# Optimization experiments

Hardware: AMD Instinct MI355X
Metric: run time of the kernel (lower is better)

Reference implementation:

```python
import jax, jax.numpy as jnp
import numpy as np

B, L, D, NH = 4, 1024, 1024, 16
DH = D // NH
H = 8 * D // 3  # SwiGLU hidden = 2730
NEG = -1e9


def setup_inputs() -> dict:
    key = jax.random.key(0)
    ks = jax.random.split(key, 8)
    init = lambda k, shape: (jax.random.normal(k, shape, jnp.float32) * 0.02)
    x = jax.random.normal(ks[0], (B, L, D), jnp.float32)
    causal = jnp.tril(jnp.ones((L, L), bool))
    m = jnp.where(causal, 0.0, NEG)[None, None].astype(jnp.float32)  # [1,1,L,L]
    return {
        'x': x,
        'm': m,
        'wx': init(ks[1], (D, 3 * D)),
        'bx': jnp.zeros((3 * D,), jnp.float32),
        'wo': init(ks[2], (D, D)),
        'bo': jnp.zeros((D,), jnp.float32),
        'mhanorm_w': jnp.ones((D,), jnp.float32),
        'ffnorm_w': jnp.ones((D,), jnp.float32),
        'u': init(ks[3], (D, H)),
        'v': init(ks[4], (D, H)),
        'w': init(ks[5], (H, D)),
    }


def rmsnorm(x, weight, eps=1e-8):
    rrms = jax.lax.rsqrt(jnp.mean(x * x, axis=-1, keepdims=True) + eps)
    return weight * x * rrms


def reference(x, m, wx, bx, wo, bo, mhanorm_w, ffnorm_w, u, v, w):
    scale = D ** (-0.5)  # note: original uses d**-0.5, NOT dh**-0.5
    qkv = rmsnorm(x, mhanorm_w) @ wx + bx                 # [B,L,3D]
    q, k, vv = jnp.split(qkv, 3, axis=-1)                  # each [B,L,D]
    split = lambda t: t.reshape(B, L, NH, DH).transpose(0, 2, 1, 3)  # [B,NH,L,DH]
    q, k, vv = split(q), split(k), split(vv)               # pe = identity (default)
    scores = jnp.einsum('bhic,bhjc->bhij', q, k) * scale + m
    A = jax.nn.softmax(scores, axis=-1)
    head = jnp.einsum('bhij,bhjc->bhic', A, vv)            # [B,NH,L,DH]
    head = head.transpose(0, 2, 1, 3).reshape(B, L, D)
    x = x + head @ wo + bo
    xn = rmsnorm(x, ffnorm_w)
    return x + (jax.nn.silu(xn @ u) * (xn @ v)) @ w
```

## Files before the change

kernel.cpp:

```cpp
#include <hip/hip_runtime.h>

#define B_  4
#define L_  1024
#define D_  1024
#define NH_ 16
#define DH_ 64
#define H_  2730
#define HP_ 2816
#define M_  4096

typedef short bf16x8 __attribute__((ext_vector_type(8)));
typedef float f32x4  __attribute__((ext_vector_type(4)));

__device__ __forceinline__ unsigned short f2bf(float f) {
    unsigned int u = __builtin_bit_cast(unsigned int, f);
    u += 0x7fffu + ((u >> 16) & 1u);
    return (unsigned short)(u >> 16);
}
__device__ __forceinline__ float bf2f(unsigned short s) {
    unsigned int u = ((unsigned int)s) << 16;
    return __builtin_bit_cast(float, u);
}

__device__ __forceinline__ void glds16(const void* g, void* l) {
    __builtin_amdgcn_global_load_lds(
        (const __attribute__((address_space(1))) unsigned int*)g,
        (__attribute__((address_space(3))) unsigned int*)l, 16, 0, 0);
}

__device__ __forceinline__ void xcd_swz(int& lx, int& ly) {
    const int gx = gridDim.x;
    const int flat = blockIdx.x + gx * blockIdx.y;
    const int r = flat & 7, q = flat >> 3;
    lx = q % gx;
    ly = r + 8 * (q / gx);
}

__global__ __launch_bounds__(256) void cvtT_rms_all(
    const float* __restrict__ wx, const float* __restrict__ wo,
    const float* __restrict__ u,  const float* __restrict__ v,
    const float* __restrict__ w,
    const float* __restrict__ x,  const float* __restrict__ mhw,
    unsigned short* __restrict__ wxb, unsigned short* __restrict__ wob,
    unsigned short* __restrict__ ub,  unsigned short* __restrict__ vb,
    unsigned short* __restrict__ wb,  unsigned short* __restrict__ xnb)
{
    __shared__ float t[32][33];
    __shared__ float red[4];
    const int id = blockIdx.x;

    if (id >= 12544) {
        const int row = id - 12544;
        const int tt = threadIdx.x;
        const float4 vv = ((const float4*)(x + (size_t)row * 1024))[tt];
        float ss = vv.x*vv.x + vv.y*vv.y + vv.z*vv.z + vv.w*vv.w;
        #pragma unroll
        for (int off = 32; off > 0; off >>= 1) ss += __shfl_down(ss, off);
        if ((tt & 63) == 0) red[tt >> 6] = ss;
        __syncthreads();
        const float tot = red[0] + red[1] + red[2] + red[3];
        const float rr = rsqrtf(tot * (1.0f / 1024.0f) + 1e-8f);
        const float4 wv = ((const float4*)mhw)[tt];
        ushort4 o;
        o.x = f2bf(vv.x * wv.x * rr); o.y = f2bf(vv.y * wv.y * rr);
        o.z = f2bf(vv.z * wv.z * rr); o.w = f2bf(vv.w * wv.w * rr);
        ((ushort4*)(xnb + (size_t)row * 1024))[tt] = o;
        return;
    }

    const float* in; unsigned short* out;
    int K, N, Kp, gx, base;
    if (id < 3072)      { in = wx; out = wxb; K = 1024; N = 3072; Kp = 1024; gx = 32; base = 0; }
    else if (id < 4096) { in = wo; out = wob; K = 1024; N = 1024; Kp = 1024; gx = 32; base = 3072; }
    else if (id < 6912) { in = u;  out = ub;  K = 1024; N = 2730; Kp = 1024; gx = 32; base = 4096; }
    else if (id < 9728) { in = v;  out = vb;  K = 1024; N = 2730; Kp = 1024; gx = 32; base = 6912; }
    else                { in = w;  out = wb;  K = 2730; N = 1024; Kp = 2816; gx = 88; base = 9728; }
    const int local = id - base;
    const int bx = local % gx, by = local / gx;

    const int k0 = bx * 32, n0 = by * 32;
    const int tx = threadIdx.x & 31, ty = threadIdx.x >> 5;
    #pragma unroll
    for (int i = 0; i < 4; ++i) {
        const int k = k0 + ty + i * 8, n = n0 + tx;
        t[ty + i * 8][tx] = (k < K && n < N) ? in[(size_t)k * N + n] : 0.0f;
    }
    __syncthreads();
    #pragma unroll
    for (int i = 0; i < 4; ++i) {
        const int n = n0 + ty + i * 8, k = k0 + tx;
        out[(size_t)n * Kp + k] = f2bf(t[tx][ty + i * 8]);
    }
}

__global__ __launch_bounds__(256) void rmsnorm_kernel(
    const float* __restrict__ x, const float* __restrict__ w,
    unsigned short* __restrict__ out)
{
    const int row = blockIdx.x;
    const int t = threadIdx.x;
    const float4 v = ((const float4*)(x + (size_t)row * 1024))[t];
    float ss = v.x*v.x + v.y*v.y + v.z*v.z + v.w*v.w;
    #pragma unroll
    for (int off = 32; off > 0; off >>= 1) ss += __shfl_down(ss, off);
    __shared__ float red[4];
    if ((t & 63) == 0) red[t >> 6] = ss;
    __syncthreads();
    const float tot = red[0] + red[1] + red[2] + red[3];
    const float rr = rsqrtf(tot * (1.0f / 1024.0f) + 1e-8f);
    const float4 wv = ((const float4*)w)[t];
    ushort4 o;
    o.x = f2bf(v.x * wv.x * rr); o.y = f2bf(v.y * wv.y * rr);
    o.z = f2bf(v.z * wv.z * rr); o.w = f2bf(v.w * wv.w * rr);
    ((ushort4*)(out + (size_t)row * 1024))[t] = o;
}

template<int EPI, int TN>
__global__ __launch_bounds__(256) void gemm_bf16(
    const unsigned short* __restrict__ A, const unsigned short* __restrict__ Bt,
    int M, int N, int K,
    const float* __restrict__ bias, const float* __restrict__ res,
    float* __restrict__ outf, unsigned short* __restrict__ outb)
{
    constexpr int NS = TN / 32;
    constexpr int G  = (TN == 128) ? 4 : 3;
    constexpr int WAIT_G = 0xF70 | G;
    __shared__ __align__(16) unsigned short As[2][128 * 32];
    __shared__ __align__(16) unsigned short Bs[2][TN * 32];
    const int tid = threadIdx.x;
    int lx, ly;
    xcd_swz(lx, ly);
    const int m0 = ly * 128, n0 = lx * TN;
    const int lane = tid & 63, w = tid >> 6;
    const int wm = w >> 1, wn = w & 1;
    const int quad = lane >> 4, l15 = lane & 15;

    f32x4 acc[4][NS] = {};

    const int p0 = w * 64 + lane;
    const int r0 = p0 >> 2, c0 = (p0 & 3) ^ ((r0 >> 1) & 3);
    const int offL0 = p0 * 8, offL1 = 2048 + p0 * 8;

    const unsigned short* Ag0 = A + (size_t)(m0 + r0) * K + c0 * 8;
    const unsigned short* Ag1 = A + (size_t)(m0 + 64 + r0) * K + c0 * 8;
    const unsigned short* Bg0 = Bt + (size_t)(n0 + r0) * K + c0 * 8;
    const unsigned short* Bg1 = Bt + (size_t)(n0 + 64 + r0) * K + c0 * 8;

    auto stage = [&](int kk, int buf) {
        glds16(Ag0 + kk, &As[buf][offL0]);
        glds16(Ag1 + kk, &As[buf][offL1]);
        glds16(Bg0 + kk, &Bs[buf][offL0]);
        if (TN == 128) glds16(Bg1 + kk, &Bs[buf][offL1]);
    };
    auto compute = [&](int buf) {
        bf16x8 af[4], bfr[NS];
        #pragma unroll
        for (int ms = 0; ms < 4; ++ms) {
            const int row = wm * 64 + ms * 16 + l15;
            af[ms] = *(const bf16x8*)&As[buf][row * 32 + ((quad ^ ((row >> 1) & 3)) * 8)];
        }
        #pragma unroll
        for (int ns = 0; ns < NS; ++ns) {
            const int row = wn * (TN / 2) + ns * 16 + l15;
            bfr[ns] = *(const bf16x8*)&Bs[buf][row * 32 + ((quad ^ ((row >> 1) & 3)) * 8)];
        }
        #pragma unroll
        for (int ms = 0; ms < 4; ++ms)
            #pragma unroll
            for (int ns = 0; ns < NS; ++ns)
                acc[ms][ns] = __builtin_amdgcn_mfma_f32_16x16x32_bf16(
                    af[ms], bfr[ns], acc[ms][ns], 0, 0, 0);
    };

    const int nk = K >> 5;
    stage(0, 0);
    for (int i = 0; i < nk; i += 2) {
        if (i + 1 < nk) { stage((i + 1) << 5, 1); __builtin_amdgcn_s_waitcnt(WAIT_G); }
        else            { __builtin_amdgcn_s_waitcnt(0xF70); }
        __builtin_amdgcn_s_barrier();
        compute(0);
        __builtin_amdgcn_s_barrier();
        if (i + 2 < nk) { stage((i + 2) << 5, 0); __builtin_amdgcn_s_waitcnt(WAIT_G); }
        else            { __builtin_amdgcn_s_waitcnt(0xF70); }
        __builtin_amdgcn_s_barrier();
        compute(1);
        __builtin_amdgcn_s_barrier();
    }

    #pragma unroll
    for (int ms = 0; ms < 4; ++ms) {
        #pragma unroll
        for (int r = 0; r < 4; ++r) {
            const int row = m0 + wm * 64 + ms * 16 + quad * 4 + r;
            const size_t ro = (size_t)row * N;
            #pragma unroll
            for (int ns = 0; ns < NS; ++ns) {
                const int col = n0 + wn * (TN / 2) + ns * 16 + l15;
                float v = acc[ms][ns][r];
                if (EPI == 0) {
                    outb[ro + col] = f2bf(v + bias[col]);
                } else if (EPI == 1) {
                    outf[ro + col] = v + bias[col] + res[ro + col];
                } else {
                    outf[ro + col] = v + res[ro + col];
                }
            }
        }
    }
}

__global__ __launch_bounds__(256, 2) void gemm_swiglu(
    const unsigned short* __restrict__ A, const unsigned short* __restrict__ Bu,
    const unsigned short* __restrict__ Bv, unsigned short* __restrict__ g)
{
    constexpr int K = 1024, N = HP_;
    constexpr int WAIT_G = 0xF76;
    __shared__ __align__(16) unsigned short As[2][128 * 32];
    __shared__ __align__(16) unsigned short Us[2][128 * 32];
    __shared__ __align__(16) unsigned short Vs[2][128 * 32];
    const int tid = threadIdx.x;
    int lx, ly;
    xcd_swz(lx, ly);
    const int m0 = ly * 128, n0 = lx * 128;
    const int lane = tid & 63, w = tid >> 6;
    const int wm = w >> 1, wn = w & 1;
    const int quad = lane >> 4, l15 = lane & 15;

    f32x4 au[4][4] = {}, av[4][4] = {};

    const int p0 = w * 64 + lane;
    const int r0 = p0 >> 2, c0 = (p0 & 3) ^ ((r0 >> 1) & 3);
    const int offL0 = p0 * 8, offL1 = 2048 + p0 * 8;

    const unsigned short* Ag0 = A  + (size_t)(m0 + r0) * K + c0 * 8;
    const unsigned short* Ag1 = A  + (size_t)(m0 + 64 + r0) * K + c0 * 8;
    const unsigned short* Ug0 = Bu + (size_t)(n0 + r0) * K + c0 * 8;
    const unsigned short* Ug1 = Bu + (size_t)(n0 + 64 + r0) * K + c0 * 8;
    const unsigned short* Vg0 = Bv + (size_t)(n0 + r0) * K + c0 * 8;
    const unsigned short* Vg1 = Bv + (size_t)(n0 + 64 + r0) * K + c0 * 8;

    auto stage = [&](int kk, int buf) {
        glds16(Ag0 + kk, &As[buf][offL0]);
        glds16(Ag1 + kk, &As[buf][offL1]);
        glds16(Ug0 + kk, &Us[buf][offL0]);
        glds16(Ug1 + kk, &Us[buf][offL1]);
        glds16(Vg0 + kk, &Vs[buf][offL0]);
        glds16(Vg1 + kk, &Vs[buf][offL1]);
    };
    auto compute = [&](int buf) {
        bf16x8 af[4], uf[4], vf[4];
        #pragma unroll
        for (int ms = 0; ms < 4; ++ms) {
            const int row = wm * 64 + ms * 16 + l15;
            af[ms] = *(const bf16x8*)&As[buf][row * 32 + ((quad ^ ((row >> 1) & 3)) * 8)];
        }
        #pragma unroll
        for (int ns = 0; ns < 4; ++ns) {
            const int row = wn * 64 + ns * 16 + l15;
            uf[ns] = *(const bf16x8*)&Us[buf][row * 32 + ((quad ^ ((row >> 1) & 3)) * 8)];
            vf[ns] = *(const bf16x8*)&Vs[buf][row * 32 + ((quad ^ ((row >> 1) & 3)) * 8)];
        }
        #pragma unroll
        for (int ms = 0; ms < 4; ++ms)
            #pragma unroll
            for (int ns = 0; ns < 4; ++ns) {
                au[ms][ns] = __builtin_amdgcn_mfma_f32_16x16x32_bf16(af[ms], uf[ns], au[ms][ns], 0, 0, 0);
                av[ms][ns] = __builtin_amdgcn_mfma_f32_16x16x32_bf16(af[ms], vf[ns], av[ms][ns], 0, 0, 0);
            }
    };

    stage(0, 0);
    for (int i = 0; i < 32; i += 2) {
        if (i + 1 < 32) { stage((i + 1) << 5, 1); __builtin_amdgcn_s_waitcnt(WAIT_G); }
        else            { __builtin_amdgcn_s_waitcnt(0xF70); }
        __builtin_amdgcn_s_barrier();
        compute(0);
        __builtin_amdgcn_s_barrier();
        if (i + 2 < 32) { stage((i + 2) << 5, 0); __builtin_amdgcn_s_waitcnt(WAIT_G); }
        else            { __builtin_amdgcn_s_waitcnt(0xF70); }
        __builtin_amdgcn_s_barrier();
        compute(1);
        __builtin_amdgcn_s_barrier();
    }

    #pragma unroll
    for (int ms = 0; ms < 4; ++ms) {
        #pragma unroll
        for (int r = 0; r < 4; ++r) {
            const int row = m0 + wm * 64 + ms * 16 + quad * 4 + r;
            const size_t ro = (size_t)row * N;
            #pragma unroll
            for (int ns = 0; ns < 4; ++ns) {
                const int col = n0 + wn * 64 + ns * 16 + l15;
                const float uu = au[ms][ns][r];
                const float vv = av[ms][ns][r];
                g[ro + col] = f2bf(uu / (1.0f + __expf(-uu)) * vv);
            }
        }
    }
}

__global__ __launch_bounds__(256) void attn_mfma2_kernel(
    const unsigned short* __restrict__ qkv, unsigned short* __restrict__ hout)
{
    __shared__ __align__(16) unsigned short Qs[64 * 72];
    __shared__ __align__(16) unsigned short Ks[2][64 * 64];
    __shared__ __align__(16) unsigned short Vt[2][64 * 72];
    __shared__ __align__(16) unsigned short Ps[64 * 68];

    const int tid = threadIdx.x;
    const int d = blockIdx.x + 8 * blockIdx.y + 128 * blockIdx.z;
    const int qa = d >> 6;
    const int hb = d & 63;
    const int h = hb & 15, b = hb >> 4;
    const int qb = 15 - qa;
    const int w = tid >> 6, lane = tid & 63;
    const int quad = lane >> 4, l15 = lane & 15;

    const size_t basek = (size_t)(b * L_) * 3072 + 1024 + h * 64;
    const size_t basev = basek + 1024;

    const int qr6 = tid >> 2, qq4 = tid & 3;
    auto stageQ = [&](int qtile) {
        const int grow = qtile * 64 + qr6;
        const unsigned short* gp = qkv + (size_t)(b * L_ + grow) * 3072 + h * 64 + qq4 * 16;
        uint4 a0 = *(const uint4*)gp;
        uint4 a1 = *(const uint4*)(gp + 8);
        unsigned short* dp = &Qs[qr6 * 72 + qq4 * 16];
        *(uint4*)dp = a0; *(uint4*)(dp + 8) = a1;
    };
    stageQ(qa);

    auto stageK = [&](int kt, int buf) {
        #pragma unroll
        for (int i = 0; i < 2; ++i) {
            const int p = i * 256 + tid;
            const int row = p >> 3;
            const int cc = (p & 7) ^ (row & 7);
            glds16(qkv + basek + (size_t)(kt * 64 + row) * 3072 + cc * 8, &Ks[buf][p * 8]);
        }
    };
    const int vkey = (tid & 31) * 2, vdp = tid >> 5;
    auto loadV = [&](int kt, uint4& v0, uint4& v1) {
        const unsigned short* gp = qkv + basev + (size_t)(kt * 64 + vkey) * 3072 + vdp * 8;
        v0 = *(const uint4*)gp;
        v1 = *(const uint4*)(gp + 3072);
    };
    auto writeV = [&](int buf, const uint4& v0, const uint4& v1) {
        union { uint4 u; unsigned short s[8]; } a, c;
        a.u = v0; c.u = v1;
        #pragma unroll
        for (int i = 0; i < 8; ++i) {
            unsigned int pk = (unsigned int)a.s[i] | ((unsigned int)c.s[i] << 16);
            *(unsigned int*)&Vt[buf][(vdp * 8 + i) * 72 + vkey] = pk;
        }
    };

    f32x4 O[4] = {};
    float l4[4] = {0.0f, 0.0f, 0.0f, 0.0f};

    stageK(0, 0);
    {
        uint4 v0, v1;
        loadV(0, v0, v1);
        writeV(0, v0, v1);
    }
    __syncthreads();

    bf16x8 af[2];
    #pragma unroll
    for (int s = 0; s < 2; ++s)
        af[s] = *(const bf16x8*)&Qs[(w * 16 + l15) * 72 + s * 32 + quad * 8];

    const float SCL2 = 0.045084220027779984f;

    int qsel = 0, kt = 0;
    for (int t = 0; t < 17; ++t) {
        if (t == qa + 1) {
            #pragma unroll
            for (int s = 0; s < 2; ++s)
                af[s] = *(const bf16x8*)&Qs[(w * 16 + l15) * 72 + s * 32 + quad * 8];
        }
        const int cb = t & 1, nb = cb ^ 1;
        const bool havenext = (t < 16);
        uint4 nv0, nv1;
        if (havenext) {
            const int ktn = (t + 1 <= qa) ? (t + 1) : (t - qa);
            stageK(ktn, nb);
            loadV(ktn, nv0, nv1);
        }

        bf16x8 bfk[4][2];
        #pragma unroll
        for (int n = 0; n < 4; ++n) {
            const int row = n * 16 + l15;
            #pragma unroll
            for (int s = 0; s < 2; ++s)
                bfk[n][s] = *(const bf16x8*)&Ks[cb][row * 64 + (((s * 4 + quad) ^ (row & 7)) * 8)];
        }
        f32x4 sacc[4] = {};
        __builtin_amdgcn_s_setprio(1);
        #pragma unroll
        for (int n = 0; n < 4; ++n) {
            sacc[n] = __builtin_amdgcn_mfma_f32_16x16x32_bf16(af[0], bfk[n][0], sacc[n], 0, 0, 0);
            sacc[n] = __builtin_amdgcn_mfma_f32_16x16x32_bf16(af[1], bfk[n][1], sacc[n], 0, 0, 0);
        }
        __builtin_amdgcn_s_setprio(0);

        const bool diag = (kt == (qsel ? qb : qa));
        float rs[4] = {0.0f, 0.0f, 0.0f, 0.0f};
        #pragma unroll
        for (int n = 0; n < 4; ++n) {
            const int col = n * 16 + l15;
            #pragma unroll
            for (int r = 0; r < 4; ++r) {
                float e = __builtin_amdgcn_exp2f(sacc[n][r] * SCL2);
                if (diag && col > (w * 16 + quad * 4 + r)) e = 0.0f;
                Ps[(w * 16 + quad * 4 + r) * 68 + col] = f2bf(e);
                rs[r] += e;
            }
        }

        if (havenext) writeV(nb, nv0, nv1);

        bf16x8 ap[2], bv[4][2];
        #pragma unroll
        for (int s = 0; s < 2; ++s)
            ap[s] = *(const bf16x8*)&Ps[(w * 16 + l15) * 68 + s * 32 + quad * 8];
        #pragma unroll
        for (int dn = 0; dn < 4; ++dn)
            #pragma unroll
            for (int s = 0; s < 2; ++s)
                bv[dn][s] = *(const bf16x8*)&Vt[cb][(dn * 16 + l15) * 72 + s * 32 + quad * 8];
        __builtin_amdgcn_s_setprio(1);
        #pragma unroll
        for (int dn = 0; dn < 4; ++dn) {
            O[dn] = __builtin_amdgcn_mfma_f32_16x16x32_bf16(ap[0], bv[dn][0], O[dn], 0, 0, 0);
            O[dn] = __builtin_amdgcn_mfma_f32_16x16x32_bf16(ap[1], bv[dn][1], O[dn], 0, 0, 0);
        }
        __builtin_amdgcn_s_setprio(0);

        #pragma unroll
        for (int r = 0; r < 4; ++r) {
            #pragma unroll
            for (int m = 1; m < 16; m <<= 1)
                rs[r] += __shfl_xor(rs[r], m);
            l4[r] += rs[r];
        }

        if (t == qa) {
            #pragma unroll
            for (int r = 0; r < 4; ++r) {
                const float inv = 1.0f / l4[r];
                const int grow = qa * 64 + w * 16 + quad * 4 + r;
                unsigned short* op = hout + (size_t)(b * L_ + grow) * 1024 + h * 64;
                #pragma unroll
                for (int dn = 0; dn < 4; ++dn)
                    op[dn * 16 + l15] = f2bf(O[dn][r] * inv);
            }
            #pragma unroll
            for (int dn = 0; dn < 4; ++dn)
                #pragma unroll
                for (int r = 0; r < 4; ++r) O[dn][r] = 0.0f;
            #pragma unroll
            for (int r = 0; r < 4; ++r) l4[r] = 0.0f;
            qsel = 1;
            kt = 0;
            stageQ(qb);
        } else {
            ++kt;
        }
        __syncthreads();
    }

    #pragma unroll
    for (int r = 0; r < 4; ++r) {
        const float inv = 1.0f / l4[r];
        const int grow = qb * 64 + w * 16 + quad * 4 + r;
        unsigned short* op = hout + (size_t)(b * L_ + grow) * 1024 + h * 64;
        #pragma unroll
        for (int dn = 0; dn < 4; ++dn)
            op[dn * 16 + l15] = f2bf(O[dn][r] * inv);
    }
}

extern "C" void kernel_launch(void* const* d_in, const int* in_sizes, int n_in,
                              void* d_out, int out_size, void* d_ws, size_t ws_size,
                              hipStream_t stream)
{
    const float* x   = (const float*)d_in[0];
    const float* wx  = (const float*)d_in[2];
    const float* bx  = (const float*)d_in[3];
    const float* wo  = (const float*)d_in[4];
    const float* bo  = (const float*)d_in[5];
    const float* mhw = (const float*)d_in[6];
    const float* ffw = (const float*)d_in[7];
    const float* u   = (const float*)d_in[8];
    const float* v   = (const float*)d_in[9];
    const float* w   = (const float*)d_in[10];
    float* out = (float*)d_out;

    char* W = (char*)d_ws;
    unsigned short* xn_bf   = (unsigned short*)(W + 0);
    unsigned short* wx_bf   = (unsigned short*)(W + 8388608);
    unsigned short* qkv_bf  = (unsigned short*)(W + 14680064);
    unsigned short* head_bf = (unsigned short*)(W + 39845888);
    unsigned short* wo_bf   = (unsigned short*)(W + 48234496);
    float*          x2      = (float*)(W + 50331648);
    unsigned short* u_bf    = (unsigned short*)(W + 67108864);
    unsigned short* v_bf    = (unsigned short*)(W + 72876032);
    unsigned short* w_bf    = (unsigned short*)(W + 78643200);
    unsigned short* g_bf    = (unsigned short*)(W + 84410368);

    cvtT_rms_all<<<16640, 256, 0, stream>>>(wx, wo, u, v, w, x, mhw,
                                            wx_bf, wo_bf, u_bf, v_bf, w_bf, xn_bf);

    gemm_bf16<0, 128><<<dim3(3072 / 128, 32), 256, 0, stream>>>(
        xn_bf, wx_bf, 4096, 3072, 1024, bx, nullptr, nullptr, qkv_bf);

    attn_mfma2_kernel<<<dim3(8, 16, 4), 256, 0, stream>>>(qkv_bf, head_bf);

    gemm_bf16<1, 64><<<dim3(1024 / 64, 32), 256, 0, stream>>>(
        head_bf, wo_bf, 4096, 1024, 1024, bo, x, x2, nullptr);

    rmsnorm_kernel<<<4096, 256, 0, stream>>>(x2, ffw, xn_bf);

    gemm_swiglu<<<dim3(2816 / 128, 32), 256, 0, stream>>>(xn_bf, u_bf, v_bf, g_bf);

    gemm_bf16<4, 64><<<dim3(1024 / 64, 32), 256, 0, stream>>>(
        g_bf, w_bf, 4096, 1024, 2816, nullptr, x2, out, nullptr);
}
```

Measured before the change: 341.1 us.

## Add K=64 tiled GEMM for N=1024 projections and regroup XCD block swizzle

Adds a gemm_k64 kernel that stages 128x64 A and 64x64 B tiles with a K depth of 64. This halves the number of barrier/staging rounds per K step compared with the previous kernel, and it is used for the output projection and the FFN down projection. The XCD swizzle is also rewritten so that each XCD gets a compact 8-row by half-width block region, which should improve L2 reuse of A rows and B columns. The new swizzle assumes a grid height of 32 and an even grid width, and it changes the block order for every GEMM that uses it. The larger LDS tiles may also reduce occupancy.

```diff
diff --git a/kernel.cpp b/kernel.cpp
--- a/kernel.cpp
+++ b/kernel.cpp
@@ -30,10 +30,11 @@
 
 __device__ __forceinline__ void xcd_swz(int& lx, int& ly) {
     const int gx = gridDim.x;
+    const int cpx = gx >> 1;
     const int flat = blockIdx.x + gx * blockIdx.y;
-    const int r = flat & 7, q = flat >> 3;
-    lx = q % gx;
-    ly = r + 8 * (q / gx);
+    const int x = flat & 7, j = flat >> 3;
+    ly = (x >> 1) * 8 + (j & 7);
+    lx = (x & 1) * cpx + (j >> 3);
 }
 
 __global__ __launch_bounds__(256) void cvtT_rms_all(
@@ -209,6 +210,110 @@
     }
 }
 
+template<int EPI>
+__global__ __launch_bounds__(256) void gemm_k64(
+    const unsigned short* __restrict__ A, const unsigned short* __restrict__ Bt,
+    int M, int N, int K,
+    const float* __restrict__ bias, const float* __restrict__ res,
+    float* __restrict__ outf, unsigned short* __restrict__ outb)
+{
+    __shared__ __align__(16) unsigned short As[2][128 * 64];
+    __shared__ __align__(16) unsigned short Bs[2][64 * 64];
+    const int tid = threadIdx.x;
+    int lx, ly;
+    xcd_swz(lx, ly);
+    const int m0 = ly * 128, n0 = lx * 64;
+    const int lane = tid & 63, w = tid >> 6;
+    const int wm = w >> 1, wn = w & 1;
+    const int quad = lane >> 4, l15 = lane & 15;
+
+    f32x4 acc[4][2] = {};
+
+    const unsigned short* Ag[4];
+    const unsigned short* Bg[2];
+    int offA[4], offB[2];
+    #pragma unroll
+    for (int i = 0; i < 4; ++i) {
+        const int p = tid + i * 256, r = p >> 3, c = (p & 7) ^ (r & 7);
+        Ag[i] = A + (size_t)(m0 + r) * K + c * 8;
+        offA[i] = p * 8;
+    }
+    #pragma unroll
+    for (int i = 0; i < 2; ++i) {
+        const int p = tid + i * 256, r = p >> 3, c = (p & 7) ^ (r & 7);
+        Bg[i] = Bt + (size_t)(n0 + r) * K + c * 8;
+        offB[i] = p * 8;
+    }
+
+    auto stage = [&](int kk, int buf) {
+        #pragma unroll
+        for (int i = 0; i < 4; ++i) glds16(Ag[i] + kk, &As[buf][offA[i]]);
+        #pragma unroll
+        for (int i = 0; i < 2; ++i) glds16(Bg[i] + kk, &Bs[buf][offB[i]]);
+    };
+    auto compute = [&](int buf) {
+        bf16x8 af[4][2], bfr[2][2];
+        #pragma unroll
+        for (int ms = 0; ms < 4; ++ms) {
+            const int row = wm * 64 + ms * 16 + l15;
+            #pragma unroll
+            for (int kk = 0; kk < 2; ++kk)
+                af[ms][kk] = *(const bf16x8*)&As[buf][row * 64 + (((kk * 4 + quad) ^ (row & 7)) * 8)];
+        }
+        #pragma unroll
+        for (int ns = 0; ns < 2; ++ns) {
+            const int row = wn * 32 + ns * 16 + l15;
+            #pragma unroll
+            for (int kk = 0; kk < 2; ++kk)
+                bfr[ns][kk] = *(const bf16x8*)&Bs[buf][row * 64 + (((kk * 4 + quad) ^ (row & 7)) * 8)];
+        }
+        #pragma unroll
+        for (int kk = 0; kk < 2; ++kk)
+            #pragma unroll
+            for (int ms = 0; ms < 4; ++ms)
+                #pragma unroll
+                for (int ns = 0; ns < 2; ++ns)
+                    acc[ms][ns] = __builtin_amdgcn_mfma_f32_16x16x32_bf16(
+                        af[ms][kk], bfr[ns][kk], acc[ms][ns], 0, 0, 0);
+    };
+
+    const int nk = K >> 6;
+    stage(0, 0);
+    for (int i = 0; i < nk; i += 2) {
+        if (i + 1 < nk) { stage((i + 1) << 6, 1); __builtin_amdgcn_s_waitcnt(0xF76); }
+        else            { __builtin_amdgcn_s_waitcnt(0xF70); }
+        __builtin_amdgcn_s_barrier();
+        compute(0);
+        __builtin_amdgcn_s_barrier();
+        if (i + 2 < nk) { stage((i + 2) << 6, 0); __builtin_amdgcn_s_waitcnt(0xF76); }
+        else            { __builtin_amdgcn_s_waitcnt(0xF70); }
+        __builtin_amdgcn_s_barrier();
+        compute(1);
+        __builtin_amdgcn_s_barrier();
+    }
+
+    #pragma unroll
+    for (int ms = 0; ms < 4; ++ms) {
+        #pragma unroll
+        for (int r = 0; r < 4; ++r) {
+            const int row = m0 + wm * 64 + ms * 16 + quad * 4 + r;
+            const size_t ro = (size_t)row * N;
+            #pragma unroll
+            for (int ns = 0; ns < 2; ++ns) {
+                const int col = n0 + wn * 32 + ns * 16 + l15;
+                float v = acc[ms][ns][r];
+                if (EPI == 0) {
+                    outb[ro + col] = f2bf(v + bias[col]);
+                } else if (EPI == 1) {
+                    outf[ro + col] = v + bias[col] + res[ro + col];
+                } else {
+                    outf[ro + col] = v + res[ro + col];
+                }
+            }
+        }
+    }
+}
+
 __global__ __launch_bounds__(256, 2) void gemm_swiglu(
     const unsigned short* __restrict__ A, const unsigned short* __restrict__ Bu,
     const unsigned short* __restrict__ Bv, unsigned short* __restrict__ g)
@@ -520,13 +625,13 @@
 
     attn_mfma2_kernel<<<dim3(8, 16, 4), 256, 0, stream>>>(qkv_bf, head_bf);
 
-    gemm_bf16<1, 64><<<dim3(1024 / 64, 32), 256, 0, stream>>>(
+    gemm_k64<1><<<dim3(1024 / 64, 32), 256, 0, stream>>>(
         head_bf, wo_bf, 4096, 1024, 1024, bo, x, x2, nullptr);
 
     rmsnorm_kernel<<<4096, 256, 0, stream>>>(x2, ffw, xn_bf);
 
     gemm_swiglu<<<dim3(2816 / 128, 32), 256, 0, stream>>>(xn_bf, u_bf, v_bf, g_bf);
 
-    gemm_bf16<4, 64><<<dim3(1024 / 64, 32), 256, 0, stream>>>(
+    gemm_k64<4><<<dim3(1024 / 64, 32), 256, 0, stream>>>(
         g_bf, w_bf, 4096, 1024, 2816, nullptr, x2, out, nullptr);
 }
```

Measured after the change: 325.4 us, median of 2. 1.05x faster.
